# Optimization experiments

Hardware: AMD Instinct MI355X
Metric: run time of the kernel (lower is better)

The kernel has to match this reference:

```python
import jax, jax.numpy as jnp
import numpy as np

UNK_ID = 0
EPS = 1e-20


def setup_inputs() -> dict:
    key = jax.random.key(0)
    k1, k2, k3, k4, k5 = jax.random.split(key, 5)
    bs, ls, vocab, emb = 8, 256, 32000, 100
    return {
        "logits": jax.random.normal(k1, (bs, ls, vocab), dtype=jnp.float32),
        "gumbel_u": jax.random.uniform(k2, (bs, ls, vocab), dtype=jnp.float32),
        "inp_word": jax.random.randint(k3, (bs, ls), 0, vocab, dtype=jnp.int64),
        "obf_mask": jax.random.randint(k4, (bs, ls), 0, 2, dtype=jnp.int32),
        "parser_emb_weight": jax.random.normal(k5, (vocab, emb), dtype=jnp.float32),
    }


def reference(logits, gumbel_u, inp_word, obf_mask, parser_emb_weight):
    # dec ends in LogSoftmax -> gen_logits are log-probs
    lp = jax.nn.log_softmax(logits, axis=-1)                       # [b,s,V]
    mask = obf_mask.astype(bool)                                   # [b,s]
    vocab = lp.shape[-1]

    # ent_loss = mean over masked rows of lp * exp(lp)
    ent_all = jnp.sum(lp * jnp.exp(lp), axis=-1)                   # [b,s]
    n_masked = jnp.sum(mask).astype(lp.dtype)
    ent_loss = jnp.sum(jnp.where(mask, ent_all, 0.0)) / (n_masked * vocab)

    # gumbel_softmax(targeted_logits, temperature=1.0) -- eval mode
    g = -jnp.log(-jnp.log(gumbel_u + EPS) + EPS)
    relaxed = jax.nn.softmax(lp + g, axis=-1)                      # [b,s,V]
    sampled_idx = jnp.argmax(relaxed, axis=-1)                     # [b,s]
    sampled_emb = jnp.einsum('bsv,vd->bsd', relaxed, parser_emb_weight)

    # masked_scatter_ chains collapse to per-position selects:
    #   masked & safe   -> sampled_idx / sampled_emb
    #   masked & unsafe -> UNK_ID / W[UNK_ID]
    #   unmasked        -> inp_word / W[inp_word]
    safe = sampled_idx != inp_word                                 # [b,s]
    obf_word = jnp.where(mask, jnp.where(safe, sampled_idx, UNK_ID), inp_word)
    base_emb = parser_emb_weight[inp_word]                         # [b,s,d]
    unk_emb = parser_emb_weight[UNK_ID]                            # [d]
    obf_word_emb = jnp.where(
        mask[..., None],
        jnp.where(safe[..., None], sampled_emb, unk_emb),
        base_emb,
    )
    return obf_word, obf_word_emb, ent_loss
```

## Files before the change

### kernel.cpp

```cpp
#include <hip/hip_runtime.h>

#define P_TOT   2048
#define V       32000
#define D       100
#define DPAD    128
#define TS      32
#define VSPLIT  10
#define KB      3200
#define VC      128
#define NCHUNK  25
#define ASTRIDE 136
#define BSTRIDE 136

typedef __attribute__((ext_vector_type(8))) short short8;
typedef __attribute__((ext_vector_type(4))) float floatx4;

static __device__ __forceinline__ unsigned short f2bf(float x) {
    unsigned u = __float_as_uint(x);
    u += 0x7FFFu + ((u >> 16) & 1u);
    return (unsigned short)(u >> 16);
}

__global__ __launch_bounds__(256)
void k_prep(const float* __restrict__ W, unsigned short* __restrict__ Wt) {
    __shared__ float tile[64 * 133];
    const int vb = blockIdx.x * 64;
    const int tid = threadIdx.x;
    #pragma unroll
    for (int it = 0; it < 32; ++it) {
        int idx = it * 256 + tid;
        int d = idx & 127, vl = idx >> 7;
        float val = (d < D) ? W[(size_t)(vb + vl) * D + d] : 0.0f;
        tile[vl * 133 + d] = val;
    }
    __syncthreads();
    #pragma unroll
    for (int it = 0; it < 32; ++it) {
        int idx = it * 256 + tid;
        int vl = idx & 63, d = idx >> 6;
        Wt[(size_t)d * V + vb + vl] = f2bf(tile[vl * 133 + d]);
    }
}

__global__ __launch_bounds__(256, 3)
void k_main(const float* __restrict__ logits, const float* __restrict__ gum,
            const unsigned short* __restrict__ Wt,
            float* __restrict__ Epart, float* __restrict__ stats) {
    __shared__ unsigned short Abuf[TS * ASTRIDE];
    __shared__ unsigned short Bbuf[DPAD * BSTRIDE];
    __shared__ __align__(16) float alphaS[TS];
    __shared__ float m2run[TS], s2run[TS], amaxv[TS];
    __shared__ int amaxi[TS];

    const int tid   = threadIdx.x;
    const int r     = tid >> 3;
    const int q     = tid & 7;
    const int lane  = tid & 63;
    const int w     = tid >> 6;
    const int mtile = w & 1;
    const int ngrp  = w >> 1;
    const int stile = blockIdx.x;
    const int vs    = blockIdx.y;

    const int grow = stile * TS + r;
    const size_t rowbase = (size_t)grow * V + (size_t)vs * KB;

    if (q == 0) {
        m2run[r] = -1e30f; s2run[r] = 0.0f;
        amaxv[r] = -1e30f; amaxi[r] = 0;
    }
    float m1 = -1e30f, sA = 0.0f, sB = 0.0f;
    floatx4 acc[4];
    #pragma unroll
    for (int i = 0; i < 4; ++i) acc[i] = (floatx4){0.f, 0.f, 0.f, 0.f};

    for (int ch = 0; ch < NCHUNK; ++ch) {
        __syncthreads();
        const int cbase = ch * VC;

        {
            const unsigned short* src = Wt + (size_t)vs * KB + cbase;
            #pragma unroll
            for (int it = 0; it < 8; ++it) {
                int idx = it * 256 + tid;
                int dd = idx >> 4, seg = idx & 15;
                uint4 vwt = *(const uint4*)(src + (size_t)dd * V + seg * 8);
                *(uint4*)(&Bbuf[dd * BSTRIDE + seg * 8]) = vwt;
            }
        }

        float lg[16], zz[16];
        {
            const float* lptr = logits + rowbase + cbase + q * 4;
            const float* uptr = gum    + rowbase + cbase + q * 4;
            float4 l4[4], u4[4];
            #pragma unroll
            for (int k = 0; k < 4; ++k) l4[k] = *(const float4*)(lptr + (size_t)k * 32);
            #pragma unroll
            for (int k = 0; k < 4; ++k) u4[k] = *(const float4*)(uptr + (size_t)k * 32);
            #pragma unroll
            for (int k = 0; k < 4; ++k) {
                lg[k*4+0] = l4[k].x; lg[k*4+1] = l4[k].y;
                lg[k*4+2] = l4[k].z; lg[k*4+3] = l4[k].w;
                float uu[4] = {u4[k].x, u4[k].y, u4[k].z, u4[k].w};
                #pragma unroll
                for (int l = 0; l < 4; ++l) {
                    float g = -logf(-logf(uu[l] + 1e-20f) + 1e-20f);
                    zz[k*4+l] = lg[k*4+l] + g;
                }
            }
        }

        {
            float cm = lg[0];
            #pragma unroll
            for (int j = 1; j < 16; ++j) cm = fmaxf(cm, lg[j]);
            float m1n = fmaxf(m1, cm);
            float sc = __expf(m1 - m1n);
            sB = (sB + sA * (m1 - m1n)) * sc;
            sA = sA * sc;
            m1 = m1n;
            #pragma unroll
            for (int j = 0; j < 16; ++j) {
                float t = lg[j] - m1;
                float e = __expf(t);
                sA += e; sB += t * e;
            }
        }

        float cmv = -1e30f; int cmi = 0;
        #pragma unroll
        for (int k = 0; k < 4; ++k)
            #pragma unroll
            for (int l = 0; l < 4; ++l) {
                int j = k*4 + l;
                int gidx = vs * KB + cbase + k*32 + q*4 + l;
                if (zz[j] > cmv) { cmv = zz[j]; cmi = gidx; }
            }
        #pragma unroll
        for (int m = 1; m < 8; m <<= 1) {
            float ov = __shfl_xor(cmv, m, 64);
            int   oi = __shfl_xor(cmi, m, 64);
            if (ov > cmv || (ov == cmv && oi < cmi)) { cmv = ov; cmi = oi; }
        }

        float m2old = m2run[r];
        float m2new = fmaxf(m2old, cmv);
        float csum = 0.0f;
        unsigned short pb[16];
        #pragma unroll
        for (int j = 0; j < 16; ++j) {
            float p = __expf(zz[j] - m2new);
            csum += p;
            pb[j] = f2bf(p);
        }
        #pragma unroll
        for (int k = 0; k < 4; ++k) {
            ushort4 v4 = make_ushort4(pb[k*4], pb[k*4+1], pb[k*4+2], pb[k*4+3]);
            *(ushort4*)(&Abuf[r * ASTRIDE + k*32 + q*4]) = v4;
        }
        #pragma unroll
        for (int m = 1; m < 8; m <<= 1) csum += __shfl_xor(csum, m, 64);
        if (q == 0) {
            float al = __expf(m2old - m2new);
            alphaS[r] = al;
            s2run[r] = s2run[r] * al + csum;
            m2run[r] = m2new;
            if (cmv > amaxv[r]) { amaxv[r] = cmv; amaxi[r] = cmi; }
        }

        __syncthreads();

        floatx4 al4 = *(const floatx4*)(&alphaS[mtile*16 + ((lane >> 4) << 2)]);
        #pragma unroll
        for (int nt = 0; nt < 4; ++nt) {
            acc[nt][0] *= al4[0]; acc[nt][1] *= al4[1];
            acc[nt][2] *= al4[2]; acc[nt][3] *= al4[3];
        }
        const int ka0 = (lane >> 4) << 3;
        const unsigned short* arow = &Abuf[(mtile*16 + (lane & 15)) * ASTRIDE + ka0];
        #pragma unroll
        for (int ks = 0; ks < 4; ++ks) {
            short8 a = *(const short8*)(arow + ks * 32);
            #pragma unroll
            for (int nt = 0; nt < 4; ++nt) {
                const unsigned short* brow =
                    &Bbuf[(ngrp*64 + nt*16 + (lane & 15)) * BSTRIDE + ka0 + ks*32];
                short8 b = *(const short8*)brow;
                acc[nt] = __builtin_amdgcn_mfma_f32_16x16x32_bf16(a, b, acc[nt], 0, 0, 0);
            }
        }
    }

    #pragma unroll
    for (int m = 1; m < 8; m <<= 1) {
        float om = __shfl_xor(m1, m, 64);
        float oA = __shfl_xor(sA, m, 64);
        float oB = __shfl_xor(sB, m, 64);
        float mn = fmaxf(m1, om);
        float ea = __expf(m1 - mn), eb = __expf(om - mn);
        sB = (sB + sA * (m1 - mn)) * ea + (oB + oA * (om - mn)) * eb;
        sA = sA * ea + oA * eb;
        m1 = mn;
    }
    if (q == 0) {
        float* st = stats + ((size_t)grow * VSPLIT + vs) * 8;
        st[0] = m1; st[1] = sA; st[2] = sB;
        st[3] = m2run[r]; st[4] = s2run[r];
        st[5] = amaxv[r]; st[6] = __int_as_float(amaxi[r]); st[7] = 0.0f;
    }
    #pragma unroll
    for (int nt = 0; nt < 4; ++nt) {
        int n = ngrp*64 + nt*16 + (lane & 15);
        if (n < D) {
            #pragma unroll
            for (int i = 0; i < 4; ++i) {
                int row = mtile*16 + ((lane >> 4) << 2) + i;
                int pos = stile * TS + row;
                Epart[((size_t)pos * VSPLIT + vs) * D + n] = acc[nt][i];
            }
        }
    }
}

__global__ __launch_bounds__(128)
void k_combine(const float* __restrict__ stats, const float* __restrict__ Epart,
               const float* __restrict__ W, const int* __restrict__ inp,
               const int* __restrict__ msk, float* __restrict__ out,
               float* __restrict__ entbuf) {
    const int pos = blockIdx.x;
    const int t = threadIdx.x;
    const float* st = stats + (size_t)pos * VSPLIT * 8;

    float m1 = -1e30f, sA = 0.0f, sB = 0.0f, m2g = -1e30f;
    float bestv = -1e30f; int besti = 0;
    #pragma unroll
    for (int p = 0; p < VSPLIT; ++p) {
        const float* s = st + p * 8;
        float om = s[0], oA = s[1], oB = s[2];
        float mn = fmaxf(m1, om);
        float ea = __expf(m1 - mn), eb = __expf(om - mn);
        sB = (sB + sA * (m1 - mn)) * ea + (oB + oA * (om - mn)) * eb;
        sA = sA * ea + oA * eb;
        m1 = mn;
        m2g = fmaxf(m2g, s[3]);
        float av = s[5];
        if (av > bestv) { bestv = av; besti = __float_as_int(s[6]); }
    }
    float beta[VSPLIT];
    float s2g = 0.0f;
    #pragma unroll
    for (int p = 0; p < VSPLIT; ++p) {
        beta[p] = __expf(st[p*8 + 3] - m2g);
        s2g += st[p*8 + 4] * beta[p];
    }

    const int iw = inp[pos];
    const bool mk = msk[pos] != 0;
    const bool safe = besti != iw;

    if (t == 0) {
        int obf = mk ? (safe ? besti : 0) : iw;
        out[pos] = (float)obf;
        float ent = sB / sA - logf(sA);
        entbuf[pos] = mk ? ent : 0.0f;
    }
    if (t < D) {
        float e = 0.0f;
        const float* ep = Epart + (size_t)pos * VSPLIT * D + t;
        #pragma unroll
        for (int p = 0; p < VSPLIT; ++p) e += ep[(size_t)p * D] * beta[p];
        e /= s2g;
        float val;
        if (mk) val = safe ? e : W[t];
        else    val = W[(size_t)iw * D + t];
        out[P_TOT + (size_t)pos * D + t] = val;
    }
}

__global__ __launch_bounds__(256)
void k_final(const float* __restrict__ entbuf, const int* __restrict__ msk,
             float* __restrict__ out) {
    __shared__ float se[4], sm[4];
    const int t = threadIdx.x;
    float e = 0.0f, m = 0.0f;
    for (int i = t; i < P_TOT; i += 256) {
        e += entbuf[i];
        m += (float)msk[i];
    }
    #pragma unroll
    for (int k = 32; k >= 1; k >>= 1) {
        e += __shfl_down(e, k, 64);
        m += __shfl_down(m, k, 64);
    }
    if ((t & 63) == 0) { se[t >> 6] = e; sm[t >> 6] = m; }
    __syncthreads();
    if (t == 0) {
        float te = se[0] + se[1] + se[2] + se[3];
        float tm = sm[0] + sm[1] + sm[2] + sm[3];
        out[P_TOT + (size_t)P_TOT * D] = te / (tm * (float)V);
    }
}

extern "C" void kernel_launch(void* const* d_in, const int* in_sizes, int n_in,
                              void* d_out, int out_size, void* d_ws, size_t ws_size,
                              hipStream_t stream) {
    const float* logits = (const float*)d_in[0];
    const float* gum    = (const float*)d_in[1];
    const int*   inp    = (const int*)d_in[2];
    const int*   msk    = (const int*)d_in[3];
    const float* W      = (const float*)d_in[4];
    float* out = (float*)d_out;

    char* ws = (char*)d_ws;
    unsigned short* Wt  = (unsigned short*)ws;
    float* Epart  = (float*)(ws + 8192000);
    float* stats  = (float*)(ws + 16384000);
    float* entbuf = (float*)(ws + 17039360);

    k_prep<<<500, 256, 0, stream>>>(W, Wt);
    dim3 g1(P_TOT / TS, VSPLIT);
    k_main<<<g1, 256, 0, stream>>>(logits, gum, Wt, Epart, stats);
    k_combine<<<P_TOT, 128, 0, stream>>>(stats, Epart, W, inp, msk, out, entbuf);
    k_final<<<1, 256, 0, stream>>>(entbuf, msk, out);
}
```

Baseline: 593.8 us.

## Halve row tile to 16 rows, keep per-row softmax state in registers

```diff
diff --git a/kernel.cpp b/kernel.cpp
--- a/kernel.cpp
+++ b/kernel.cpp
@@ -4,7 +4,7 @@
 #define V       32000
 #define D       100
 #define DPAD    128
-#define TS      32
+#define TS      16
 #define VSPLIT  10
 #define KB      3200
 #define VC      128
@@ -17,8 +17,7 @@
 
 static __device__ __forceinline__ unsigned short f2bf(float x) {
     unsigned u = __float_as_uint(x);
-    u += 0x7FFFu + ((u >> 16) & 1u);
-    return (unsigned short)(u >> 16);
+    return (unsigned short)((u + 0x8000u) >> 16);
 }
 
 __global__ __launch_bounds__(256)
@@ -38,41 +37,39 @@
     for (int it = 0; it < 32; ++it) {
         int idx = it * 256 + tid;
         int vl = idx & 63, d = idx >> 6;
-        Wt[(size_t)d * V + vb + vl] = f2bf(tile[vl * 133 + d]);
-    }
-}
-
-__global__ __launch_bounds__(256, 3)
+        unsigned u = __float_as_uint(tile[vl * 133 + d]);
+        u += 0x7FFFu + ((u >> 16) & 1u);
+        Wt[(size_t)d * V + vb + vl] = (unsigned short)(u >> 16);
+    }
+}
+
+__global__ __launch_bounds__(256, 4)
 void k_main(const float* __restrict__ logits, const float* __restrict__ gum,
             const unsigned short* __restrict__ Wt,
             float* __restrict__ Epart, float* __restrict__ stats) {
     __shared__ unsigned short Abuf[TS * ASTRIDE];
     __shared__ unsigned short Bbuf[DPAD * BSTRIDE];
     __shared__ __align__(16) float alphaS[TS];
-    __shared__ float m2run[TS], s2run[TS], amaxv[TS];
-    __shared__ int amaxi[TS];
 
     const int tid   = threadIdx.x;
-    const int r     = tid >> 3;
-    const int q     = tid & 7;
+    const int r     = tid >> 4;
+    const int q     = tid & 15;
     const int lane  = tid & 63;
     const int w     = tid >> 6;
-    const int mtile = w & 1;
-    const int ngrp  = w >> 1;
+    const int quad  = lane >> 4;
+    const int l16   = lane & 15;
     const int stile = blockIdx.x;
     const int vs    = blockIdx.y;
 
     const int grow = stile * TS + r;
     const size_t rowbase = (size_t)grow * V + (size_t)vs * KB;
 
-    if (q == 0) {
-        m2run[r] = -1e30f; s2run[r] = 0.0f;
-        amaxv[r] = -1e30f; amaxi[r] = 0;
-    }
     float m1 = -1e30f, sA = 0.0f, sB = 0.0f;
-    floatx4 acc[4];
-    #pragma unroll
-    for (int i = 0; i < 4; ++i) acc[i] = (floatx4){0.f, 0.f, 0.f, 0.f};
+    float m2 = -1e30f, s2 = 0.0f;
+    float rmaxv = -1e30f; int rmaxi = 0;
+    floatx4 acc[2];
+    acc[0] = (floatx4){0.f,0.f,0.f,0.f};
+    acc[1] = (floatx4){0.f,0.f,0.f,0.f};
 
     for (int ch = 0; ch < NCHUNK; ++ch) {
         __syncthreads();
@@ -89,39 +86,31 @@
             }
         }
 
-        float lg[16], zz[16];
-        {
-            const float* lptr = logits + rowbase + cbase + q * 4;
-            const float* uptr = gum    + rowbase + cbase + q * 4;
-            float4 l4[4], u4[4];
-            #pragma unroll
-            for (int k = 0; k < 4; ++k) l4[k] = *(const float4*)(lptr + (size_t)k * 32);
-            #pragma unroll
-            for (int k = 0; k < 4; ++k) u4[k] = *(const float4*)(uptr + (size_t)k * 32);
-            #pragma unroll
-            for (int k = 0; k < 4; ++k) {
-                lg[k*4+0] = l4[k].x; lg[k*4+1] = l4[k].y;
-                lg[k*4+2] = l4[k].z; lg[k*4+3] = l4[k].w;
-                float uu[4] = {u4[k].x, u4[k].y, u4[k].z, u4[k].w};
-                #pragma unroll
-                for (int l = 0; l < 4; ++l) {
-                    float g = -logf(-logf(uu[l] + 1e-20f) + 1e-20f);
-                    zz[k*4+l] = lg[k*4+l] + g;
-                }
+        float lg[8], zz[8];
+        #pragma unroll
+        for (int k = 0; k < 2; ++k) {
+            float4 l4 = *(const float4*)(logits + rowbase + cbase + k*64 + q*4);
+            float4 u4 = *(const float4*)(gum    + rowbase + cbase + k*64 + q*4);
+            lg[k*4+0] = l4.x; lg[k*4+1] = l4.y; lg[k*4+2] = l4.z; lg[k*4+3] = l4.w;
+            float uu[4] = {u4.x, u4.y, u4.z, u4.w};
+            #pragma unroll
+            for (int l = 0; l < 4; ++l) {
+                float g = -__logf(-__logf(uu[l] + 1e-20f) + 1e-20f);
+                zz[k*4+l] = lg[k*4+l] + g;
             }
         }
 
         {
             float cm = lg[0];
             #pragma unroll
-            for (int j = 1; j < 16; ++j) cm = fmaxf(cm, lg[j]);
+            for (int j = 1; j < 8; ++j) cm = fmaxf(cm, lg[j]);
             float m1n = fmaxf(m1, cm);
             float sc = __expf(m1 - m1n);
             sB = (sB + sA * (m1 - m1n)) * sc;
             sA = sA * sc;
             m1 = m1n;
             #pragma unroll
-            for (int j = 0; j < 16; ++j) {
+            for (int j = 0; j < 8; ++j) {
                 float t = lg[j] - m1;
                 float e = __expf(t);
                 sA += e; sB += t * e;
@@ -130,62 +119,58 @@
 
         float cmv = -1e30f; int cmi = 0;
         #pragma unroll
-        for (int k = 0; k < 4; ++k)
+        for (int k = 0; k < 2; ++k)
             #pragma unroll
             for (int l = 0; l < 4; ++l) {
                 int j = k*4 + l;
-                int gidx = vs * KB + cbase + k*32 + q*4 + l;
+                int gidx = vs * KB + cbase + k*64 + q*4 + l;
                 if (zz[j] > cmv) { cmv = zz[j]; cmi = gidx; }
             }
         #pragma unroll
-        for (int m = 1; m < 8; m <<= 1) {
+        for (int m = 1; m < 16; m <<= 1) {
             float ov = __shfl_xor(cmv, m, 64);
             int   oi = __shfl_xor(cmi, m, 64);
             if (ov > cmv || (ov == cmv && oi < cmi)) { cmv = ov; cmi = oi; }
         }
-
-        float m2old = m2run[r];
-        float m2new = fmaxf(m2old, cmv);
+        if (cmv > rmaxv) { rmaxv = cmv; rmaxi = cmi; }
+
+        float m2new = fmaxf(m2, cmv);
         float csum = 0.0f;
-        unsigned short pb[16];
-        #pragma unroll
-        for (int j = 0; j < 16; ++j) {
+        unsigned short pb[8];
+        #pragma unroll
+        for (int j = 0; j < 8; ++j) {
             float p = __expf(zz[j] - m2new);
             csum += p;
             pb[j] = f2bf(p);
         }
         #pragma unroll
-        for (int k = 0; k < 4; ++k) {
+        for (int k = 0; k < 2; ++k) {
             ushort4 v4 = make_ushort4(pb[k*4], pb[k*4+1], pb[k*4+2], pb[k*4+3]);
-            *(ushort4*)(&Abuf[r * ASTRIDE + k*32 + q*4]) = v4;
-        }
-        #pragma unroll
-        for (int m = 1; m < 8; m <<= 1) csum += __shfl_xor(csum, m, 64);
-        if (q == 0) {
-            float al = __expf(m2old - m2new);
-            alphaS[r] = al;
-            s2run[r] = s2run[r] * al + csum;
-            m2run[r] = m2new;
-            if (cmv > amaxv[r]) { amaxv[r] = cmv; amaxi[r] = cmi; }
-        }
+            *(ushort4*)(&Abuf[r * ASTRIDE + k*64 + q*4]) = v4;
+        }
+        #pragma unroll
+        for (int m = 1; m < 16; m <<= 1) csum += __shfl_xor(csum, m, 64);
+        float al = __expf(m2 - m2new);
+        s2 = s2 * al + csum;
+        m2 = m2new;
+        if (q == 0) alphaS[r] = al;
 
         __syncthreads();
 
-        floatx4 al4 = *(const floatx4*)(&alphaS[mtile*16 + ((lane >> 4) << 2)]);
-        #pragma unroll
-        for (int nt = 0; nt < 4; ++nt) {
+        floatx4 al4 = *(const floatx4*)(&alphaS[quad << 2]);
+        #pragma unroll
+        for (int nt = 0; nt < 2; ++nt) {
             acc[nt][0] *= al4[0]; acc[nt][1] *= al4[1];
             acc[nt][2] *= al4[2]; acc[nt][3] *= al4[3];
         }
-        const int ka0 = (lane >> 4) << 3;
-        const unsigned short* arow = &Abuf[(mtile*16 + (lane & 15)) * ASTRIDE + ka0];
+        const unsigned short* arow = &Abuf[l16 * ASTRIDE + (quad << 3)];
         #pragma unroll
         for (int ks = 0; ks < 4; ++ks) {
             short8 a = *(const short8*)(arow + ks * 32);
             #pragma unroll
-            for (int nt = 0; nt < 4; ++nt) {
+            for (int nt = 0; nt < 2; ++nt) {
                 const unsigned short* brow =
-                    &Bbuf[(ngrp*64 + nt*16 + (lane & 15)) * BSTRIDE + ka0 + ks*32];
+                    &Bbuf[(w*32 + nt*16 + l16) * BSTRIDE + (quad << 3) + ks*32];
                 short8 b = *(const short8*)brow;
                 acc[nt] = __builtin_amdgcn_mfma_f32_16x16x32_bf16(a, b, acc[nt], 0, 0, 0);
             }
@@ -193,7 +178,7 @@
     }
 
     #pragma unroll
-    for (int m = 1; m < 8; m <<= 1) {
+    for (int m = 1; m < 16; m <<= 1) {
         float om = __shfl_xor(m1, m, 64);
         float oA = __shfl_xor(sA, m, 64);
         float oB = __shfl_xor(sB, m, 64);
@@ -206,17 +191,16 @@
     if (q == 0) {
         float* st = stats + ((size_t)grow * VSPLIT + vs) * 8;
         st[0] = m1; st[1] = sA; st[2] = sB;
-        st[3] = m2run[r]; st[4] = s2run[r];
-        st[5] = amaxv[r]; st[6] = __int_as_float(amaxi[r]); st[7] = 0.0f;
-    }
-    #pragma unroll
-    for (int nt = 0; nt < 4; ++nt) {
-        int n = ngrp*64 + nt*16 + (lane & 15);
+        st[3] = m2; st[4] = s2;
+        st[5] = rmaxv; st[6] = __int_as_float(rmaxi); st[7] = 0.0f;
+    }
+    #pragma unroll
+    for (int nt = 0; nt < 2; ++nt) {
+        int n = w*32 + nt*16 + l16;
         if (n < D) {
             #pragma unroll
             for (int i = 0; i < 4; ++i) {
-                int row = mtile*16 + ((lane >> 4) << 2) + i;
-                int pos = stile * TS + row;
+                int pos = stile * TS + (quad << 2) + i;
                 Epart[((size_t)pos * VSPLIT + vs) * D + n] = acc[nt][i];
             }
         }
```

New measurement: 594.8 us. About the same (+0.2%).
